# Kernel optimization log

Hardware: AMD Instinct MI355X
Metric: run time of the kernel (lower is better)

Reference implementation:

```python
import jax, jax.numpy as jnp
import numpy as np

NH, HD, MBS = 32, 64, 16   # num_heads, head_dim, mini_batch_size
BASE_LR = 1.0
ROPE_BASE = 10000.0
EPS = 1e-6


def _rotate_half(x):
    x1, x2 = jnp.split(x, 2, axis=-1)
    return jnp.concatenate((-x2, x1), axis=-1)


def _permute_qk(x):
    B, H, L, D = x.shape
    return x.reshape(B, H, L, D // 2, 2).swapaxes(-1, -2).reshape(B, H, L, D)


def _undo_permute_qk(x):
    B, H, L, D = x.shape
    return x.reshape(B, H, L, 2, D // 2).swapaxes(-1, -2).reshape(B, H, L, D)


def _ln_fwd(x, gamma, beta):
    mu = x.mean(-1, keepdims=True)
    var = x.var(-1, keepdims=True)
    return gamma * ((x - mu) / jnp.sqrt(var + EPS)) + beta


def _ln_fused_l2_bwd(x, target, gamma, beta):
    # grad of 0.5*||LN(x) - target||^2 wrt x, fused
    D = x.shape[-1]
    mu = x.mean(-1, keepdims=True)
    std = jnp.sqrt(x.var(-1, keepdims=True) + EPS)
    x_hat = (x - mu) / std
    y = gamma * x_hat + beta
    g = (y - target) * gamma
    return (D * g - g.sum(-1, keepdims=True) - x_hat * (g * x_hat).sum(-1, keepdims=True)) / (D * std)


def setup_inputs() -> dict:
    key = jax.random.key(0)
    ks = jax.random.split(key, 8)
    B, L, C, OUT = 4, 2048, 2048, 768
    s = 0.02
    return {
        "hidden_states": jax.random.normal(ks[0], (B, L, C), jnp.float32),
        "position_ids": jnp.broadcast_to(jnp.arange(L, dtype=jnp.int32)[None], (B, L)),
        "Wq": jax.random.normal(ks[1], (C, C), jnp.float32) * s,
        "Wk": jax.random.normal(ks[2], (C, C), jnp.float32) * s,
        "Wv": jax.random.normal(ks[3], (C, C), jnp.float32) * s,
        "Wo": jax.random.normal(ks[4], (C, OUT), jnp.float32) * s,
        "W1": jax.random.normal(ks[5], (NH, HD, HD), jnp.float32) * s,
        "b1": jnp.zeros((NH, 1, HD), jnp.float32),
        "ttt_lr_weight": jax.random.normal(ks[6], (NH, 1, C), jnp.float32) * s,
        "ttt_lr_bias": jnp.zeros((NH, 1), jnp.float32),
        "learnable_token_idx": jnp.zeros((MBS,), jnp.float32),
        "ttt_norm_weight": jnp.ones((NH, HD), jnp.float32),
        "ttt_norm_bias": jnp.zeros((NH, HD), jnp.float32),
        "post_norm_weight": jnp.ones((C,), jnp.float32),
        "post_norm_bias": jnp.zeros((C,), jnp.float32),
    }


def reference(hidden_states, position_ids, Wq, Wk, Wv, Wo, W1, b1,
              ttt_lr_weight, ttt_lr_bias, learnable_token_idx,
              ttt_norm_weight, ttt_norm_bias, post_norm_weight, post_norm_bias):
    B, L, C = hidden_states.shape
    NM = L // MBS
    # QKV projections -> [B, NH, L, HD]
    XQ = (hidden_states @ Wq).reshape(B, L, NH, HD).transpose(0, 2, 1, 3)
    XK = (hidden_states @ Wk).reshape(B, L, NH, HD).transpose(0, 2, 1, 3)
    XV = (hidden_states @ Wv).reshape(B, L, NH, HD).transpose(0, 2, 1, 3)
    # RoPE on positions modulo the mini-batch size
    pos = (position_ids % MBS).astype(jnp.float32)  # [B, L]
    inv_freq = 1.0 / (ROPE_BASE ** (jnp.arange(0, HD, 2, dtype=jnp.float32) / HD))
    freqs = pos[..., None] * inv_freq               # [B, L, HD/2]
    emb = jnp.concatenate((freqs, freqs), axis=-1)  # [B, L, HD]
    cos = jnp.cos(emb)[:, None]                     # [B, 1, L, HD]
    sin = jnp.sin(emb)[:, None]
    XQ, XK = _permute_qk(XQ), _permute_qk(XK)
    XQ = XQ * cos + _rotate_half(XQ) * sin
    XK = XK * cos + _rotate_half(XK) * sin
    XQ, XK = _undo_permute_qk(XQ), _undo_permute_qk(XK)
    # reshape into mini-batches: [B, NH, NM, K, HD]
    X = hidden_states.reshape(B, NM, MBS, C)
    XQ = XQ.reshape(B, NH, NM, MBS, HD)
    XK = XK.reshape(B, NH, NM, MBS, HD)
    XV = XV.reshape(B, NH, NM, MBS, HD)
    # eta: per-token learnable LR gate
    ttt_lr = jax.nn.sigmoid(
        jnp.einsum('bnkc,hdc->bhnkd', X, ttt_lr_weight)
        + ttt_lr_bias.reshape(1, NH, 1, 1, 1))              # [B,NH,NM,K,1]
    ttt_lr_eta = BASE_LR * ttt_lr.transpose(0, 1, 2, 4, 3) / HD  # [B,NH,NM,1,K]
    token_idx = jnp.clip(1.0 / jnp.arange(1, MBS + 1, dtype=jnp.float32)
                         + learnable_token_idx, 0.0, None)
    token_eta = token_idx.reshape(1, 1, 1, MBS, 1)
    eta = token_eta * ttt_lr_eta                            # [B,NH,NM,K,K]
    # TTT-Linear dual-form mini-batch scan
    ln_w = ttt_norm_weight.reshape(1, NH, 1, HD)
    ln_b = ttt_norm_bias.reshape(1, NH, 1, HD)
    W1_0 = jnp.broadcast_to(W1[None], (B, NH, HD, HD))
    b1_0 = jnp.broadcast_to(b1[None], (B, NH, 1, HD))
    tril = jnp.tril(jnp.ones((MBS, MBS), hidden_states.dtype))

    def step(carry, xs):
        W1_s, b1_s = carry
        xq, xk, xv, eta_m = xs                 # [B,NH,K,HD], eta_m [B,NH,K,K]
        Z1 = xk @ W1_s + b1_s
        target = xv - xk
        grad = _ln_fused_l2_bwd(Z1, target, ln_w, ln_b)
        Attn = tril * (xq @ xk.swapaxes(-1, -2))
        b1_bar = b1_s - (tril * eta_m) @ grad
        Z1_bar = xq @ W1_s - (eta_m * Attn) @ grad + b1_bar
        last_eta = eta_m[:, :, -1, :, None]    # [B,NH,K,1]
        W1_new = W1_s - (last_eta * xk).swapaxes(-1, -2) @ grad
        b1_new = b1_s - jnp.sum(last_eta * grad, axis=-2, keepdims=True)
        out = xq + _ln_fwd(Z1_bar, ln_w, ln_b)
        return (W1_new, b1_new), out

    xs = (XQ.transpose(2, 0, 1, 3, 4), XK.transpose(2, 0, 1, 3, 4),
          XV.transpose(2, 0, 1, 3, 4), eta.transpose(2, 0, 1, 3, 4))
    _, outs = jax.lax.scan(step, (W1_0, b1_0), xs)   # [NM,B,NH,K,HD]
    out = outs.transpose(1, 2, 0, 3, 4).reshape(B, NH, L, HD)
    out = out.transpose(0, 2, 1, 3).reshape(B, L, C)
    # post LayerNorm (eps 1e-6) and output projection
    mu = out.mean(-1, keepdims=True)
    var = out.var(-1, keepdims=True)
    out = (out - mu) / jnp.sqrt(var + EPS) * post_norm_weight + post_norm_bias
    return out @ Wo
```

## Files before the change

### kernel.cpp

```cpp
#include <hip/hip_runtime.h>
#include <cstddef>
#include <cstdint>

#define B_DIM   4
#define L_SEQ   2048
#define C_DIM   2048
#define OUT_DIM 768
#define NHEADS  32
#define HDIM    64
#define MBS_    16
#define NMINI   128
#define EPS_    1e-6f

typedef _Float16 half8 __attribute__((ext_vector_type(8)));
typedef _Float16 half4 __attribute__((ext_vector_type(4)));
typedef float floatx4 __attribute__((ext_vector_type(4)));

__device__ __forceinline__ void glds16(const void* g, void* l) {
    __builtin_amdgcn_global_load_lds(
        (const __attribute__((address_space(1))) uint32_t*)g,
        (__attribute__((address_space(3))) uint32_t*)l, 16, 0, 0);
}

__device__ __forceinline__ void split8(const float4 a, const float4 b,
                                       half8& hi, half8& lo) {
    const float x[8] = {a.x, a.y, a.z, a.w, b.x, b.y, b.z, b.w};
#pragma unroll
    for (int e = 0; e < 8; e++) {
        const _Float16 h = (_Float16)x[e];
        hi[e] = h;
        lo[e] = (_Float16)(x[e] - (float)h);
    }
}

__device__ __forceinline__ void split4(const float4 a, half4& hi, half4& lo) {
    const float x[4] = {a.x, a.y, a.z, a.w};
#pragma unroll
    for (int e = 0; e < 4; e++) {
        const _Float16 h = (_Float16)x[e];
        hi[e] = h;
        lo[e] = (_Float16)(x[e] - (float)h);
    }
}

__device__ __forceinline__ uint32_t pack_hl(float v) {
    const _Float16 h = (_Float16)v;
    const _Float16 l = (_Float16)(v - (float)h);
    union { _Float16 f[2]; uint32_t u; } p;
    p.f[0] = h; p.f[1] = l;
    return p.u;
}

__device__ __forceinline__ half8 pairswap(half8 v) {
    union { half8 h; uint32_t u[4]; } a, b;
    a.h = v;
#pragma unroll
    for (int e = 0; e < 4; e++) b.u[e] = (a.u[e] >> 16) | (a.u[e] << 16);
    return b.h;
}

template<int CTRL>
__device__ __forceinline__ float dpp_add(float v) {
    const int x = __builtin_amdgcn_update_dpp(0, __float_as_int(v), CTRL, 0xF, 0xF, false);
    return v + __int_as_float(x);
}
__device__ __forceinline__ float red16(float v) {
    v = dpp_add<0xB1>(v);
    v = dpp_add<0x4E>(v);
    v = dpp_add<0x124>(v);
    v = dpp_add<0x128>(v);
    return v;
}

__device__ __forceinline__ void bar_lgkm() {
    asm volatile("s_waitcnt lgkmcnt(0)\n\ts_barrier" ::: "memory");
}

__global__ __launch_bounds__(256)
void asplit_kernel(const float* __restrict__ A, _Float16* __restrict__ Ahi,
                   _Float16* __restrict__ Alo)
{
    const size_t idx = ((size_t)blockIdx.x * 256 + threadIdx.x) * 16;
    half8 h0, l0, h1, l1;
    {
        const float4 a = *(const float4*)(A + idx);
        const float4 b = *(const float4*)(A + idx + 4);
        split8(a, b, h0, l0);
    }
    {
        const float4 a = *(const float4*)(A + idx + 8);
        const float4 b = *(const float4*)(A + idx + 12);
        split8(a, b, h1, l1);
    }
    *(half8*)(Ahi + idx)     = h0;
    *(half8*)(Ahi + idx + 8) = h1;
    *(half8*)(Alo + idx)     = l0;
    *(half8*)(Alo + idx + 8) = l1;
}

template<int APRE>
__global__ __launch_bounds__(256)
void gemm_t(const float* __restrict__ A32,
            const _Float16* __restrict__ Ahi, const _Float16* __restrict__ Alo,
            const _Float16* __restrict__ Bhi, const _Float16* __restrict__ Blo,
            float* __restrict__ Cout, int mode, int doRope)
{
    __shared__ __align__(16) float    sA[APRE ? 1 : 4096];
    __shared__ __align__(16) _Float16 sAh[APRE ? 4096 : 1];
    __shared__ __align__(16) _Float16 sAl[APRE ? 4096 : 1];
    __shared__ __align__(16) _Float16 sBhi[4096];
    __shared__ __align__(16) _Float16 sBlo[4096];
    const int tid = threadIdx.x;
    const int nwg = gridDim.x * gridDim.y;
    int lin = blockIdx.y * gridDim.x + blockIdx.x;
    lin = (lin & 7) * (nwg >> 3) + (lin >> 3);
    const int m0 = (lin / gridDim.x) * 128;
    const int n0 = (lin % gridDim.x) * 128;
    const int K = 2048;

    size_t gA[4]; float* lA[4];
    size_t gAs[2]; _Float16 *lAh[2], *lAl[2];
    if constexpr (!APRE) {
#pragma unroll
        for (int I = 0; I < 4; I++) {
            const int c = I * 256 + tid;
            const int row = c >> 3, seg = (c & 7) ^ (row & 7);
            gA[I] = (size_t)(m0 + row) * K + seg * 4;
            lA[I] = &sA[c * 4];
        }
    } else {
#pragma unroll
        for (int I = 0; I < 2; I++) {
            const int c = I * 256 + tid;
            const int row = c >> 2, seg = (c & 3) ^ ((row >> 1) & 3);
            gAs[I] = (size_t)(m0 + row) * K + seg * 8;
            lAh[I] = &sAh[c * 8];
            lAl[I] = &sAl[c * 8];
        }
    }
    size_t gB[2]; _Float16 *lBh[2], *lBl[2];
#pragma unroll
    for (int I = 0; I < 2; I++) {
        const int c = I * 256 + tid;
        const int row = c >> 2, seg = (c & 3) ^ ((row >> 1) & 3);
        gB[I] = (size_t)(n0 + row) * K + seg * 8;
        lBh[I] = &sBhi[c * 8];
        lBl[I] = &sBlo[c * 8];
    }

    const int lane = tid & 63, quad = lane >> 4, lc = lane & 15;
    const int wv = tid >> 6, wm = wv & 1, wn = wv >> 1;
    int offA0[4], offA1[4], offAp[4], offB[4];
#pragma unroll
    for (int i = 0; i < 4; i++) {
        const int rA = wm * 64 + i * 16 + lc;
        if constexpr (!APRE) {
            offA0[i] = (rA * 8 + ((2 * quad)     ^ (rA & 7))) * 4;
            offA1[i] = (rA * 8 + ((2 * quad + 1) ^ (rA & 7))) * 4;
        } else {
            offAp[i] = (rA * 4 + (quad ^ ((rA >> 1) & 3))) * 8;
        }
    }
#pragma unroll
    for (int j = 0; j < 4; j++) {
        const int rB = wn * 64 + j * 16 + lc;
        offB[j] = (rB * 4 + (quad ^ ((rB >> 1) & 3))) * 8;
    }

    floatx4 acc[4][4];
#pragma unroll
    for (int i = 0; i < 4; i++)
#pragma unroll
        for (int j = 0; j < 4; j++) acc[i][j] = (floatx4)0.0f;

    for (int k0 = 0; k0 < K; k0 += 32) {
        __syncthreads();
        if constexpr (!APRE) {
#pragma unroll
            for (int I = 0; I < 4; I++) glds16(A32 + gA[I] + k0, lA[I]);
        } else {
#pragma unroll
            for (int I = 0; I < 2; I++) {
                glds16(Ahi + gAs[I] + k0, lAh[I]);
                glds16(Alo + gAs[I] + k0, lAl[I]);
            }
        }
#pragma unroll
        for (int I = 0; I < 2; I++) {
            glds16(Bhi + gB[I] + k0, lBh[I]);
            glds16(Blo + gB[I] + k0, lBl[I]);
        }
        __syncthreads();

        half8 ah[4], al[4], bh[4], bl[4];
#pragma unroll
        for (int i = 0; i < 4; i++) {
            if constexpr (!APRE) {
                const float4 va = *(const float4*)&sA[offA0[i]];
                const float4 vb = *(const float4*)&sA[offA1[i]];
                split8(va, vb, ah[i], al[i]);
            } else {
                ah[i] = *(const half8*)&sAh[offAp[i]];
                al[i] = *(const half8*)&sAl[offAp[i]];
            }
        }
#pragma unroll
        for (int j = 0; j < 4; j++) {
            bh[j] = *(const half8*)&sBhi[offB[j]];
            bl[j] = *(const half8*)&sBlo[offB[j]];
        }
#pragma unroll
        for (int i = 0; i < 4; i++)
#pragma unroll
            for (int j = 0; j < 4; j++) {
                acc[i][j] = __builtin_amdgcn_mfma_f32_16x16x32_f16(ah[i], bh[j], acc[i][j], 0, 0, 0);
                acc[i][j] = __builtin_amdgcn_mfma_f32_16x16x32_f16(ah[i], bl[j], acc[i][j], 0, 0, 0);
                acc[i][j] = __builtin_amdgcn_mfma_f32_16x16x32_f16(al[i], bh[j], acc[i][j], 0, 0, 0);
            }
    }

    float cs[4][4], sn[4][4];
    if (doRope) {
#pragma unroll
        for (int j = 0; j < 4; j++) {
            const int ii = ((j * 16 + lc) & 63) >> 1;
            const float invf = expf(-(float)ii * 0.28782313662425574f);
#pragma unroll
            for (int r = 0; r < 4; r++) {
                const float ang = (float)(quad * 4 + r) * invf;
                sincosf(ang, &sn[j][r], &cs[j][r]);
            }
        }
    }
    const int oddcol = lc & 1;
#pragma unroll
    for (int i = 0; i < 4; i++) {
#pragma unroll
        for (int j = 0; j < 4; j++) {
            floatx4 v = acc[i][j];
            if (doRope) {
#pragma unroll
                for (int r = 0; r < 4; r++) {
                    const float partner = __shfl_xor(v[r], 1);
                    v[r] = v[r] * cs[j][r] + partner * (oddcol ? sn[j][r] : -sn[j][r]);
                }
            }
            const int n = n0 + wn * 64 + j * 16 + lc;
            if (mode == 0) {
                const int h = (n >> 6) & 31, d = n & 63;
#pragma unroll
                for (int r = 0; r < 4; r++) {
                    const int m = m0 + wm * 64 + i * 16 + quad * 4 + r;
                    const int b = m >> 11, li = m & 2047;
                    Cout[((size_t)(b * 32 + h) * 2048 + li) * 64 + d] = v[r];
                }
            } else {
#pragma unroll
                for (int r = 0; r < 4; r++) {
                    const int m = m0 + wm * 64 + i * 16 + quad * 4 + r;
                    Cout[(size_t)m * OUT_DIM + n] = v[r];
                }
            }
        }
    }
}

__global__ __launch_bounds__(256)
void wtrans_kernel(const float* __restrict__ W, _Float16* __restrict__ BThi,
                   _Float16* __restrict__ BTlo, int Nw)
{
    __shared__ float tile[32][33];
    const int t = threadIdx.x, tx = t & 31, ty = t >> 5;
    const int n0 = blockIdx.x * 32, k0 = blockIdx.y * 32;
    const int K = 2048;
#pragma unroll
    for (int r = 0; r < 4; r++)
        tile[ty + r * 8][tx] = W[(size_t)(k0 + ty + r * 8) * Nw + n0 + tx];
    __syncthreads();
#pragma unroll
    for (int r = 0; r < 4; r++) {
        const float val = tile[tx][ty + r * 8];
        const _Float16 hh = (_Float16)val;
        const size_t o = (size_t)(n0 + ty + r * 8) * K + k0 + tx;
        BThi[o] = hh;
        BTlo[o] = (_Float16)(val - (float)hh);
    }
}

__global__ __launch_bounds__(256)
void lr_kernel(const float* __restrict__ hidden, const float* __restrict__ wlr,
               const float* __restrict__ lr_bias, float* __restrict__ lrs)
{
    __shared__ float sRow[2048];
    __shared__ float sPart[32][9];
    const int m = blockIdx.x;
    const int t = threadIdx.x;
    const float* row = hidden + (size_t)m * C_DIM;
#pragma unroll
    for (int j = 0; j < 8; j++) sRow[t + j * 256] = row[t + j * 256];
    __syncthreads();
    const int h = t >> 3, p = t & 7;
    const float* w = wlr + (size_t)h * C_DIM;
    float s = 0.0f;
#pragma unroll 8
    for (int k = 0; k < 64; k++) {
        const int c = k * 32 + p * 4;
        const float4 a = *(const float4*)(sRow + c);
        const float4 b = *(const float4*)(w + c);
        s += a.x * b.x + a.y * b.y + a.z * b.z + a.w * b.w;
    }
    sPart[h][p] = s;
    __syncthreads();
    if (t < 32) {
        float v = 0.0f;
#pragma unroll
        for (int p2 = 0; p2 < 8; p2++) v += sPart[t][p2];
        v += lr_bias[t];
        const float sig = 1.0f / (1.0f + expf(-v));
        lrs[((size_t)(m >> 11) * NHEADS + t) * L_SEQ + (m & 2047)] = sig;
    }
}

__global__ __launch_bounds__(256, 1)
void scan_mfma(const float* __restrict__ XQ, const float* __restrict__ XK,
               float* __restrict__ XVo, const float* __restrict__ LRS,
               const float* __restrict__ W1i, const float* __restrict__ b1i,
               const float* __restrict__ lt, const float* __restrict__ lnw,
               const float* __restrict__ lnb)
{
    __shared__ __align__(16) _Float16 sXqH[1024], sXqL[1024];
    __shared__ __align__(16) _Float16 sXkH[1024], sXkL[1024];
    __shared__ __align__(16) float    sTgt[16 * 68];
    __shared__ __align__(16) float    sXq32[2][16 * 68];
    __shared__ __align__(16) _Float16 sW1H[4096], sW1L[4096];
    __shared__ __align__(16) uint32_t sKT[64 * 20];
    __shared__ __align__(16) uint32_t sCf[16 * 20];
    __shared__ __align__(16) float sRedA[16 * 36];
    __shared__ __align__(16) float sRedC[16 * 12];
    __shared__ __align__(16) float sEta[16];
    __shared__ float sB1[64];

    const int bh = blockIdx.x, h = bh & 31;
    const int t = threadIdx.x;
    const int lane = t & 63, q = lane >> 4, lc = lane & 15;
    const int w = t >> 6;
    const int col = w * 16 + lc;
    const int iRow = t >> 4;
    const int m = t & 15;

    if (t < 64) sB1[t] = b1i[h * 64 + t];

    float w1s[4][4];
#pragma unroll
    for (int t4 = 0; t4 < 4; t4++)
#pragma unroll
        for (int r = 0; r < 4; r++) {
            const float v = W1i[h * 4096 + (16 * t4 + lc) * 64 + (16 * w + 4 * q + r)];
            w1s[t4][r] = v;
            const int nn = 16 * w + 4 * q + r, k = 16 * t4 + lc;
            const int off = nn * 64 + ((((k >> 3) ^ (nn & 7)) << 3) | (k & 7));
            const _Float16 hh = (_Float16)v;
            sW1H[off] = hh; sW1L[off] = (_Float16)(v - (float)hh);
        }

    const float gamC = lnw[h * 64 + col], betC = lnb[h * 64 + col];
    const float g2c = gamC * gamC;
    float sumG2 = 0.0f;
#pragma unroll
    for (int d0 = 0; d0 < 16; d0++) {
        const float4 gv = *(const float4*)(lnw + h * 64 + d0 * 4);
        sumG2 += gv.x * gv.x + gv.y * gv.y + gv.z * gv.z + gv.w * gv.w;
    }
    float tokR[4];
#pragma unroll
    for (int r = 0; r < 4; r++)
        tokR[r] = fmaxf(1.0f / (float)(4 * q + r + 1) + lt[4 * q + r], 0.0f);
    const float tok15 = fmaxf(1.0f / 16.0f + lt[15], 0.0f);

    __syncthreads();

    const size_t base = (size_t)bh * L_SEQ * HDIM;
    const float* xq_g = XQ + base;
    const float* xk_g = XK + base;
    float* xv_g = XVo + base;
    const float* lr_g = LRS + (size_t)bh * L_SEQ;

    float4 cq = *(const float4*)(xq_g + t * 4);
    float4 ck = *(const float4*)(xk_g + t * 4);
    float4 cv = *(const float4*)(xv_g + t * 4);
    float clr = lr_g[m];

    const int rw = 16 * w + lc;
    const int stOff = iRow * 64 + ((((m >> 1) ^ (iRow & 7)) << 3) | ((m & 1) << 2));
    const int gkm = (m ^ (m >> 2)) & 3;
    const int ktWb = 4 * (w ^ gkm) + q;

    for (int n = 0; n < NMINI; n++) {
        const int buf = n & 1;
        {
            half4 hq, lq, hk, lk;
            split4(cq, hq, lq);
            split4(ck, hk, lk);
            *(half4*)&sXqH[stOff] = hq;
            *(half4*)&sXqL[stOff] = lq;
            *(half4*)&sXkH[stOff] = hk;
            *(half4*)&sXkL[stOff] = lk;
            const float4 tg = make_float4(cv.x - ck.x, cv.y - ck.y,
                                          cv.z - ck.z, cv.w - ck.w);
            *(float4*)&sTgt[iRow * 68 + m * 4] = tg;
            *(float4*)&sXq32[buf][iRow * 68 + m * 4] = cq;
            const float kvv[4] = {ck.x, ck.y, ck.z, ck.w};
#pragma unroll
            for (int i2 = 0; i2 < 4; i2++)
                sKT[(4 * m + i2) * 20 + ktWb] = pack_hl(kvv[i2]);
        }
        if (t < 16) sEta[t] = clr * (1.0f / 64.0f);
        const int np = (n + 1) & (NMINI - 1);
        const float4 nq = *(const float4*)(xq_g + np * 1024 + t * 4);
        const float4 nk = *(const float4*)(xk_g + np * 1024 + t * 4);
        const float4 nv = *(const float4*)(xv_g + np * 1024 + t * 4);
        const float nlr = lr_g[np * 16 + m];
        bar_lgkm();

        const float b1c = sB1[col];
        const float4 ev = *(const float4*)&sEta[4 * q];
        const float evv[4] = {ev.x, ev.y, ev.z, ev.w};

        half8 qh[2], ql[2], kh[2], kl[2], wh[2], wl[2];
#pragma unroll
        for (int f = 0; f < 2; f++) {
            const int cx = ((4 * f + q) ^ (lc & 7)) << 3;
            qh[f] = *(const half8*)&sXqH[lc * 64 + cx];
            ql[f] = *(const half8*)&sXqL[lc * 64 + cx];
            kh[f] = *(const half8*)&sXkH[lc * 64 + cx];
            kl[f] = *(const half8*)&sXkL[lc * 64 + cx];
            const int cw = ((4 * f + q) ^ (rw & 7)) << 3;
            wh[f] = *(const half8*)&sW1H[rw * 64 + cw];
            wl[f] = *(const half8*)&sW1L[rw * 64 + cw];
        }

        floatx4 z1a = (floatx4)0.0f, zba = (floatx4)0.0f, at = (floatx4)0.0f;
#pragma unroll
        for (int f = 0; f < 2; f++) {
            z1a = __builtin_amdgcn_mfma_f32_16x16x32_f16(kh[f], wh[f], z1a, 0, 0, 0);
            z1a = __builtin_amdgcn_mfma_f32_16x16x32_f16(kh[f], wl[f], z1a, 0, 0, 0);
            z1a = __builtin_amdgcn_mfma_f32_16x16x32_f16(kl[f], wh[f], z1a, 0, 0, 0);
            zba = __builtin_amdgcn_mfma_f32_16x16x32_f16(qh[f], wh[f], zba, 0, 0, 0);
            zba = __builtin_amdgcn_mfma_f32_16x16x32_f16(qh[f], wl[f], zba, 0, 0, 0);
            zba = __builtin_amdgcn_mfma_f32_16x16x32_f16(ql[f], wh[f], zba, 0, 0, 0);
        }
        if (w == 0) {
            const float etaLC = sEta[lc];
#pragma unroll
            for (int f = 0; f < 2; f++) {
                at = __builtin_amdgcn_mfma_f32_16x16x32_f16(qh[f], kh[f], at, 0, 0, 0);
                at = __builtin_amdgcn_mfma_f32_16x16x32_f16(qh[f], kl[f], at, 0, 0, 0);
                at = __builtin_amdgcn_mfma_f32_16x16x32_f16(ql[f], kh[f], at, 0, 0, 0);
            }
#pragma unroll
            for (int r = 0; r < 4; r++) {
                const int i = 4 * q + r;
                const float cfv = (lc <= i) ? -tokR[r] * etaLC * (at[r] + 1.0f) : 0.0f;
                sCf[i * 20 + 4 * ((lc >> 2) ^ q) + (lc & 3)] = pack_hl(cfv);
            }
        }

        float z[4], cE[4];
        float sz[4], szz[4], sgz[4], sgzz[4], sc[4], scz[4];
#pragma unroll
        for (int r = 0; r < 4; r++) {
            const int row = 4 * q + r;
            z[r] = z1a[r] + b1c;
            const float tgt = sTgt[row * 68 + col];
            cE[r] = gamC * (betC - tgt);
            const float zz = z[r] * z[r];
            sz[r]   = red16(z[r]);
            szz[r]  = red16(zz);
            sgz[r]  = red16(g2c * z[r]);
            sgzz[r] = red16(g2c * zz);
            sc[r]   = red16(cE[r]);
            scz[r]  = red16(cE[r] * z[r]);
        }
        if (lc == 0) {
#pragma unroll
            for (int r = 0; r < 4; r++) {
                const int rb = (4 * q + r) * 36;
                sRedA[rb + 0  + w] = sz[r];
                sRedA[rb + 4  + w] = szz[r];
                sRedA[rb + 8  + w] = sgz[r];
                sRedA[rb + 12 + w] = sgzz[r];
                sRedA[rb + 16 + w] = sc[r];
                sRedA[rb + 20 + w] = scz[r];
            }
        }
        bar_lgkm();

        half8 ktp[4];
#pragma unroll
        for (int t4 = 0; t4 < 4; t4++) {
            const int gkr = ((lc >> 2) ^ t4) & 3;
            ktp[t4] = *(const half8*)&sKT[(16 * t4 + lc) * 20 + 4 * (q ^ gkr)];
        }
        const half8 cfp = *(const half8*)&sCf[lc * 20 + 4 * (q ^ (lc >> 2))];

        float gr[4];
#pragma unroll
        for (int r = 0; r < 4; r++) {
            const int rb = (4 * q + r) * 36;
            const float4 a0 = *(const float4*)&sRedA[rb + 0];
            const float4 a1 = *(const float4*)&sRedA[rb + 4];
            const float4 a2 = *(const float4*)&sRedA[rb + 8];
            const float4 a3 = *(const float4*)&sRedA[rb + 12];
            const float4 a4 = *(const float4*)&sRedA[rb + 16];
            const float4 a5 = *(const float4*)&sRedA[rb + 20];
            const float Sz   = a0.x + a0.y + a0.z + a0.w;
            const float Szz  = a1.x + a1.y + a1.z + a1.w;
            const float Sgz  = a2.x + a2.y + a2.z + a2.w;
            const float Sgzz = a3.x + a3.y + a3.z + a3.w;
            const float Sc   = a4.x + a4.y + a4.z + a4.w;
            const float Scz  = a5.x + a5.y + a5.z + a5.w;
            const float mu  = Sz * (1.0f / 64.0f);
            const float ex2 = Szz * (1.0f / 64.0f);
            const float rs  = rsqrtf(ex2 - mu * mu + EPS_);
            const float G1 = rs * (Sgz - mu * sumG2) + Sc;
            const float G2 = rs * rs * (Sgzz - 2.0f * mu * Sgz + mu * mu * sumG2)
                           + rs * (Scz - mu * Sc);
            const float xh = (z[r] - mu) * rs;
            const float g  = g2c * xh + cE[r];
            gr[r] = (64.0f * g - G1 - xh * G2) * rs * (1.0f / 64.0f);
        }

        half8 gf, gfl;
#pragma unroll
        for (int r = 0; r < 4; r++) {
            const _Float16 h0 = (_Float16)gr[r];
            gf[2 * r]     = h0;
            gf[2 * r + 1] = (_Float16)(gr[r] - (float)h0);
            const float gl = gr[r] * (tok15 * evv[r]);
            const _Float16 h1 = (_Float16)gl;
            gfl[2 * r]     = h1;
            gfl[2 * r + 1] = (_Float16)(gl - (float)h1);
        }
        const half8 gfs  = pairswap(gf);
        const half8 gfls = pairswap(gfl);

        zba = __builtin_amdgcn_mfma_f32_16x16x32_f16(cfp, gf,  zba, 0, 0, 0);
        zba = __builtin_amdgcn_mfma_f32_16x16x32_f16(cfp, gfs, zba, 0, 0, 0);
#pragma unroll
        for (int t4 = 0; t4 < 4; t4++) {
            floatx4 up = (floatx4)0.0f;
            up = __builtin_amdgcn_mfma_f32_16x16x32_f16(gfl,  ktp[t4], up, 0, 0, 0);
            up = __builtin_amdgcn_mfma_f32_16x16x32_f16(gfls, ktp[t4], up, 0, 0, 0);
#pragma unroll
            for (int r = 0; r < 4; r++) w1s[t4][r] -= up[r];
        }

        float z2[4], p1[4], p2[4];
#pragma unroll
        for (int r = 0; r < 4; r++) {
            z2[r] = zba[r] + b1c;
            p1[r] = red16(z2[r]);
            p2[r] = red16(z2[r] * z2[r]);
        }
        if (lc == 0)
#pragma unroll
            for (int r = 0; r < 4; r++) {
                const int rb = (4 * q + r) * 12;
                sRedC[rb + w]     = p1[r];
                sRedC[rb + 4 + w] = p2[r];
            }

        {
            float p = gr[0] * evv[0] + gr[1] * evv[1] + gr[2] * evv[2] + gr[3] * evv[3];
            p += __shfl_xor(p, 16);
            p += __shfl_xor(p, 32);
            if (q == 0) sB1[col] -= tok15 * p;
        }
#pragma unroll
        for (int t4 = 0; t4 < 4; t4++)
#pragma unroll
            for (int r = 0; r < 4; r++) {
                const int nn = 16 * w + 4 * q + r, k = 16 * t4 + lc;
                const int off = nn * 64 + ((((k >> 3) ^ (nn & 7)) << 3) | (k & 7));
                const float v = w1s[t4][r];
                const _Float16 hh = (_Float16)v;
                sW1H[off] = hh; sW1L[off] = (_Float16)(v - (float)hh);
            }
        bar_lgkm();

#pragma unroll
        for (int r = 0; r < 4; r++) {
            const int row = 4 * q + r;
            const float4 a = *(const float4*)&sRedC[row * 12];
            const float4 b = *(const float4*)&sRedC[row * 12 + 4];
            const float mu  = (a.x + a.y + a.z + a.w) * (1.0f / 64.0f);
            const float ex2 = (b.x + b.y + b.z + b.w) * (1.0f / 64.0f);
            const float rs  = rsqrtf(ex2 - mu * mu + EPS_);
            const float xqv = sXq32[buf][row * 68 + col];
            xv_g[n * 1024 + row * 64 + col] = xqv + gamC * ((z2[r] - mu) * rs) + betC;
        }
        cq = nq; ck = nk; cv = nv; clr = nlr;
    }
}

__global__ __launch_bounds__(256)
void postln_kernel(const float* __restrict__ Ob, const float* __restrict__ pnw,
                   const float* __restrict__ pnb, _Float16* __restrict__ XNhi,
                   _Float16* __restrict__ XNlo)
{
    const int m = blockIdx.x;
    const int b = m >> 11, l = m & 2047;
    const int t = threadIdx.x;
    float v[8];
    float s1 = 0.0f, s2 = 0.0f;
    const int c0 = t * 8;
    const int hh = c0 >> 6, d0 = c0 & 63;
    const float* bas = Ob + (size_t)b * NHEADS * L_SEQ * HDIM + (size_t)l * HDIM
                     + (size_t)hh * (L_SEQ * HDIM) + d0;
    {
        const float4 va = *(const float4*)(bas);
        const float4 vb = *(const float4*)(bas + 4);
        v[0] = va.x; v[1] = va.y; v[2] = va.z; v[3] = va.w;
        v[4] = vb.x; v[5] = vb.y; v[6] = vb.z; v[7] = vb.w;
    }
#pragma unroll
    for (int j = 0; j < 8; j++) { s1 += v[j]; s2 += v[j] * v[j]; }
#pragma unroll
    for (int o = 1; o < 64; o <<= 1) { s1 += __shfl_xor(s1, o); s2 += __shfl_xor(s2, o); }
    __shared__ float r1[4], r2[4];
    const int w = t >> 6;
    if ((t & 63) == 0) { r1[w] = s1; r2[w] = s2; }
    __syncthreads();
    s1 = r1[0] + r1[1] + r1[2] + r1[3];
    s2 = r2[0] + r2[1] + r2[2] + r2[3];
    const float mu = s1 * (1.0f / 2048.0f);
    const float var = s2 * (1.0f / 2048.0f) - mu * mu;
    const float rstd = rsqrtf(var + EPS_);
    half8 oh, ol;
#pragma unroll
    for (int j = 0; j < 8; j++) {
        const float y = (v[j] - mu) * rstd * pnw[c0 + j] + pnb[c0 + j];
        const _Float16 hy = (_Float16)y;
        oh[j] = hy;
        ol[j] = (_Float16)(y - (float)hy);
    }
    *(half8*)(XNhi + (size_t)m * C_DIM + c0) = oh;
    *(half8*)(XNlo + (size_t)m * C_DIM + c0) = ol;
}

extern "C" void kernel_launch(void* const* d_in, const int* in_sizes, int n_in,
                              void* d_out, int out_size, void* d_ws, size_t ws_size,
                              hipStream_t stream)
{
    (void)in_sizes; (void)n_in; (void)out_size;
    const float* hidden  = (const float*)d_in[0];
    const float* Wq      = (const float*)d_in[2];
    const float* Wk      = (const float*)d_in[3];
    const float* Wv      = (const float*)d_in[4];
    const float* Wo      = (const float*)d_in[5];
    const float* W1      = (const float*)d_in[6];
    const float* b1      = (const float*)d_in[7];
    const float* wlr     = (const float*)d_in[8];
    const float* lr_bias = (const float*)d_in[9];
    const float* lt      = (const float*)d_in[10];
    const float* lnw     = (const float*)d_in[11];
    const float* lnb     = (const float*)d_in[12];
    const float* pnw     = (const float*)d_in[13];
    const float* pnb     = (const float*)d_in[14];

    const size_t TEN = (size_t)B_DIM * NHEADS * L_SEQ * HDIM;
    float* XQ  = (float*)d_ws;
    float* XK  = XQ + TEN;
    float* XVo = XK + TEN;
    float* LRS = XVo + TEN;
    _Float16* Ahi = (_Float16*)(LRS + 262144);
    _Float16* Alo = Ahi + TEN;
    const size_t needBytes = (3 * TEN + 262144) * 4 + TEN * 4;
    const int useAsplit = (ws_size >= needBytes) ? 1 : 0;
    const dim3 blk(256);

    _Float16* BThi = (_Float16*)d_out;
    _Float16* BTlo = BThi + (size_t)C_DIM * C_DIM;

    lr_kernel<<<dim3(B_DIM * L_SEQ), blk, 0, stream>>>(hidden, wlr, lr_bias, LRS);
    if (useAsplit)
        asplit_kernel<<<dim3(4096), blk, 0, stream>>>(hidden, Ahi, Alo);

    const float* Wmats[3] = {Wq, Wk, Wv};
    float* outs[3] = {XQ, XK, XVo};
    for (int p = 0; p < 3; p++) {
        wtrans_kernel<<<dim3(64, 64), blk, 0, stream>>>(Wmats[p], BThi, BTlo, C_DIM);
        if (useAsplit)
            gemm_t<1><<<dim3(16, 64), blk, 0, stream>>>(nullptr, Ahi, Alo,
                                                        BThi, BTlo, outs[p],
                                                        0, (p < 2) ? 1 : 0);
        else
            gemm_t<0><<<dim3(16, 64), blk, 0, stream>>>(hidden, nullptr, nullptr,
                                                        BThi, BTlo, outs[p],
                                                        0, (p < 2) ? 1 : 0);
    }
    scan_mfma<<<dim3(B_DIM * NHEADS), blk, 0, stream>>>(XQ, XK, XVo, LRS,
                                                        W1, b1, lt, lnw, lnb);
    _Float16* XNhi = (_Float16*)XQ;
    _Float16* XNlo = XNhi + TEN;
    _Float16* WThi = (_Float16*)XVo;
    WThi = (_Float16*)XK;
    _Float16* WTlo = WThi + (size_t)OUT_DIM * C_DIM;
    postln_kernel<<<dim3(B_DIM * L_SEQ), blk, 0, stream>>>(XVo, pnw, pnb,
                                                           XNhi, XNlo);
    wtrans_kernel<<<dim3(24, 64), blk, 0, stream>>>(Wo, WThi, WTlo, OUT_DIM);
    gemm_t<1><<<dim3(6, 64), blk, 0, stream>>>(nullptr, XNhi, XNlo,
                                               WThi, WTlo, (float*)d_out, 1, 0);
}
```

Baseline: 1.401 ms.

## Add triple-buffered 256x128 split-fp16 GEMM with 512 threads for projections

Replaces the pre-split fp16 GEMM path with a new gemm8 kernel. It uses 512-thread blocks computing 256x128 tiles and a three-stage LDS ring buffer, so global-to-LDS loads for step t+2 are issued while MFMAs run on step t. It waits with explicit vmcnt and barrier instructions and raises wave priority around the MFMA block. The goal is to hide global load latency and cut the per-iteration double syncthreads, at the cost of much more LDS (about 144KB), which limits occupancy to one block per CU.

```diff
diff --git a/kernel.cpp b/kernel.cpp
--- a/kernel.cpp
+++ b/kernel.cpp
@@ -98,45 +98,189 @@
     *(half8*)(Alo + idx + 8) = l1;
 }
 
-template<int APRE>
+__global__ __launch_bounds__(512)
+void gemm8(const _Float16* __restrict__ Ahi, const _Float16* __restrict__ Alo,
+           const _Float16* __restrict__ Bhi, const _Float16* __restrict__ Blo,
+           float* __restrict__ Cout, int Ndim, int mode, int doRope)
+{
+    __shared__ __align__(16) _Float16 sAh[3][8192];
+    __shared__ __align__(16) _Float16 sAl[3][8192];
+    __shared__ __align__(16) _Float16 sBh[3][4096];
+    __shared__ __align__(16) _Float16 sBl[3][4096];
+    const int tid = threadIdx.x;
+    const int nbx = Ndim >> 7;
+    const int nwg = gridDim.x;
+    int lin = blockIdx.x;
+    lin = (lin & 7) * (nwg >> 3) + (lin >> 3);
+    const int m0 = (lin / nbx) * 256;
+    const int n0 = (lin % nbx) * 128;
+    const int K = 2048;
+
+    size_t gA[2];
+    int lA[2];
+#pragma unroll
+    for (int X = 0; X < 2; X++) {
+        const int c = X * 512 + tid;
+        const int row = c >> 2, s = c & 3;
+        const int ks = s ^ ((row >> 1) & 3);
+        gA[X] = (size_t)(m0 + row) * K + ks * 8;
+        lA[X] = c * 8;
+    }
+    size_t gB;
+    int lB;
+    {
+        const int row = tid >> 2, s = tid & 3;
+        const int ks = s ^ ((row >> 1) & 3);
+        gB = (size_t)(n0 + row) * K + ks * 8;
+        lB = tid * 8;
+    }
+
+    const int lane = tid & 63, q = lane >> 4, lc = lane & 15;
+    const int w = tid >> 6, wm = w >> 1, wn = w & 1;
+    int offA[4], offB[4];
+#pragma unroll
+    for (int i = 0; i < 4; i++) {
+        const int rA = wm * 64 + i * 16 + lc;
+        offA[i] = rA * 32 + ((q ^ ((rA >> 1) & 3)) << 3);
+    }
+#pragma unroll
+    for (int j = 0; j < 4; j++) {
+        const int rB = wn * 64 + j * 16 + lc;
+        offB[j] = rB * 32 + ((q ^ ((rB >> 1) & 3)) << 3);
+    }
+
+    floatx4 acc[4][4];
+#pragma unroll
+    for (int i = 0; i < 4; i++)
+#pragma unroll
+        for (int j = 0; j < 4; j++) acc[i][j] = (floatx4)0.0f;
+
+#define STAGE(T)                                                         \
+    {                                                                    \
+        const int b_ = (T) % 3;                                          \
+        const int ko_ = (T) * 32;                                        \
+        glds16(Ahi + gA[0] + ko_, &sAh[b_][lA[0]]);                      \
+        glds16(Alo + gA[0] + ko_, &sAl[b_][lA[0]]);                      \
+        glds16(Ahi + gA[1] + ko_, &sAh[b_][lA[1]]);                      \
+        glds16(Alo + gA[1] + ko_, &sAl[b_][lA[1]]);                      \
+        glds16(Bhi + gB + ko_,    &sBh[b_][lB]);                         \
+        glds16(Blo + gB + ko_,    &sBl[b_][lB]);                         \
+    }
+
+#define FRAGS(B_)                                                        \
+    half8 ah[4], al[4], bh[4], bl[4];                                    \
+    _Pragma("unroll")                                                    \
+    for (int i = 0; i < 4; i++) {                                        \
+        ah[i] = *(const half8*)&sAh[B_][offA[i]];                        \
+        al[i] = *(const half8*)&sAl[B_][offA[i]];                        \
+    }                                                                    \
+    _Pragma("unroll")                                                    \
+    for (int j = 0; j < 4; j++) {                                        \
+        bh[j] = *(const half8*)&sBh[B_][offB[j]];                        \
+        bl[j] = *(const half8*)&sBl[B_][offB[j]];                        \
+    }
+
+#define MFMAS                                                            \
+    __builtin_amdgcn_s_setprio(1);                                       \
+    _Pragma("unroll")                                                    \
+    for (int i = 0; i < 4; i++)                                          \
+        _Pragma("unroll")                                                \
+        for (int j = 0; j < 4; j++) {                                    \
+            acc[i][j] = __builtin_amdgcn_mfma_f32_16x16x32_f16(ah[i], bh[j], acc[i][j], 0, 0, 0); \
+            acc[i][j] = __builtin_amdgcn_mfma_f32_16x16x32_f16(ah[i], bl[j], acc[i][j], 0, 0, 0); \
+            acc[i][j] = __builtin_amdgcn_mfma_f32_16x16x32_f16(al[i], bh[j], acc[i][j], 0, 0, 0); \
+        }                                                                \
+    __builtin_amdgcn_s_setprio(0);
+
+    STAGE(0)
+    STAGE(1)
+    asm volatile("s_waitcnt vmcnt(6) lgkmcnt(0)\n\ts_barrier" ::: "memory");
+
+    for (int t = 0; t < 62; t++) {
+        const int b = t % 3;
+        FRAGS(b)
+        STAGE(t + 2)
+        MFMAS
+        asm volatile("s_waitcnt vmcnt(6) lgkmcnt(0)\n\ts_barrier" ::: "memory");
+    }
+    {
+        FRAGS(2)
+        MFMAS
+        asm volatile("s_waitcnt vmcnt(0) lgkmcnt(0)\n\ts_barrier" ::: "memory");
+    }
+    {
+        FRAGS(0)
+        MFMAS
+    }
+#undef STAGE
+#undef FRAGS
+#undef MFMAS
+
+    float cs[4][4], sn[4][4];
+    if (doRope) {
+#pragma unroll
+        for (int j = 0; j < 4; j++) {
+            const int ii = ((j * 16 + lc) & 63) >> 1;
+            const float invf = expf(-(float)ii * 0.28782313662425574f);
+#pragma unroll
+            for (int r = 0; r < 4; r++) {
+                const float ang = (float)(q * 4 + r) * invf;
+                sincosf(ang, &sn[j][r], &cs[j][r]);
+            }
+        }
+    }
+    const int oddcol = lc & 1;
+#pragma unroll
+    for (int i = 0; i < 4; i++) {
+#pragma unroll
+        for (int j = 0; j < 4; j++) {
+            floatx4 v = acc[i][j];
+            if (doRope) {
+#pragma unroll
+                for (int r = 0; r < 4; r++) {
+                    const float partner = __shfl_xor(v[r], 1);
+                    v[r] = v[r] * cs[j][r] + partner * (oddcol ? sn[j][r] : -sn[j][r]);
+                }
+            }
+            const int n = n0 + wn * 64 + j * 16 + lc;
+            if (mode == 0) {
+                const int h = (n >> 6) & 31, d = n & 63;
+#pragma unroll
+                for (int r = 0; r < 4; r++) {
+                    const int m = m0 + wm * 64 + i * 16 + q * 4 + r;
+                    const int b = m >> 11, li = m & 2047;
+                    Cout[((size_t)(b * 32 + h) * 2048 + li) * 64 + d] = v[r];
+                }
+            } else {
+#pragma unroll
+                for (int r = 0; r < 4; r++) {
+                    const int m = m0 + wm * 64 + i * 16 + q * 4 + r;
+                    Cout[(size_t)m * OUT_DIM + n] = v[r];
+                }
+            }
+        }
+    }
+}
+
 __global__ __launch_bounds__(256)
-void gemm_t(const float* __restrict__ A32,
-            const _Float16* __restrict__ Ahi, const _Float16* __restrict__ Alo,
-            const _Float16* __restrict__ Bhi, const _Float16* __restrict__ Blo,
-            float* __restrict__ Cout, int mode, int doRope)
+void gemm_f32(const float* __restrict__ A,
+              const _Float16* __restrict__ Bhi, const _Float16* __restrict__ Blo,
+              float* __restrict__ Cout, int mode, int doRope)
 {
-    __shared__ __align__(16) float    sA[APRE ? 1 : 4096];
-    __shared__ __align__(16) _Float16 sAh[APRE ? 4096 : 1];
-    __shared__ __align__(16) _Float16 sAl[APRE ? 4096 : 1];
+    __shared__ __align__(16) float    sA[4096];
     __shared__ __align__(16) _Float16 sBhi[4096];
     __shared__ __align__(16) _Float16 sBlo[4096];
     const int tid = threadIdx.x;
-    const int nwg = gridDim.x * gridDim.y;
-    int lin = blockIdx.y * gridDim.x + blockIdx.x;
-    lin = (lin & 7) * (nwg >> 3) + (lin >> 3);
-    const int m0 = (lin / gridDim.x) * 128;
-    const int n0 = (lin % gridDim.x) * 128;
+    const int m0 = blockIdx.y * 128, n0 = blockIdx.x * 128;
     const int K = 2048;
 
     size_t gA[4]; float* lA[4];
-    size_t gAs[2]; _Float16 *lAh[2], *lAl[2];
-    if constexpr (!APRE) {
-#pragma unroll
-        for (int I = 0; I < 4; I++) {
-            const int c = I * 256 + tid;
-            const int row = c >> 3, seg = (c & 7) ^ (row & 7);
-            gA[I] = (size_t)(m0 + row) * K + seg * 4;
-            lA[I] = &sA[c * 4];
-        }
-    } else {
-#pragma unroll
-        for (int I = 0; I < 2; I++) {
-            const int c = I * 256 + tid;
-            const int row = c >> 2, seg = (c & 3) ^ ((row >> 1) & 3);
-            gAs[I] = (size_t)(m0 + row) * K + seg * 8;
-            lAh[I] = &sAh[c * 8];
-            lAl[I] = &sAl[c * 8];
-        }
+#pragma unroll
+    for (int I = 0; I < 4; I++) {
+        const int c = I * 256 + tid;
+        const int row = c >> 3, seg = (c & 7) ^ (row & 7);
+        gA[I] = (size_t)(m0 + row) * K + seg * 4;
+        lA[I] = &sA[c * 4];
     }
     size_t gB[2]; _Float16 *lBh[2], *lBl[2];
 #pragma unroll
@@ -150,16 +294,12 @@
 
     const int lane = tid & 63, quad = lane >> 4, lc = lane & 15;
     const int wv = tid >> 6, wm = wv & 1, wn = wv >> 1;
-    int offA0[4], offA1[4], offAp[4], offB[4];
+    int offA0[4], offA1[4], offB[4];
 #pragma unroll
     for (int i = 0; i < 4; i++) {
         const int rA = wm * 64 + i * 16 + lc;
-        if constexpr (!APRE) {
-            offA0[i] = (rA * 8 + ((2 * quad)     ^ (rA & 7))) * 4;
-            offA1[i] = (rA * 8 + ((2 * quad + 1) ^ (rA & 7))) * 4;
-        } else {
-            offAp[i] = (rA * 4 + (quad ^ ((rA >> 1) & 3))) * 8;
-        }
+        offA0[i] = (rA * 8 + ((2 * quad)     ^ (rA & 7))) * 4;
+        offA1[i] = (rA * 8 + ((2 * quad + 1) ^ (rA & 7))) * 4;
     }
 #pragma unroll
     for (int j = 0; j < 4; j++) {
@@ -175,16 +315,8 @@
 
     for (int k0 = 0; k0 < K; k0 += 32) {
         __syncthreads();
-        if constexpr (!APRE) {
-#pragma unroll
-            for (int I = 0; I < 4; I++) glds16(A32 + gA[I] + k0, lA[I]);
-        } else {
-#pragma unroll
-            for (int I = 0; I < 2; I++) {
-                glds16(Ahi + gAs[I] + k0, lAh[I]);
-                glds16(Alo + gAs[I] + k0, lAl[I]);
-            }
-        }
+#pragma unroll
+        for (int I = 0; I < 4; I++) glds16(A + gA[I] + k0, lA[I]);
 #pragma unroll
         for (int I = 0; I < 2; I++) {
             glds16(Bhi + gB[I] + k0, lBh[I]);
@@ -195,14 +327,9 @@
         half8 ah[4], al[4], bh[4], bl[4];
 #pragma unroll
         for (int i = 0; i < 4; i++) {
-            if constexpr (!APRE) {
-                const float4 va = *(const float4*)&sA[offA0[i]];
-                const float4 vb = *(const float4*)&sA[offA1[i]];
-                split8(va, vb, ah[i], al[i]);
-            } else {
-                ah[i] = *(const half8*)&sAh[offAp[i]];
-                al[i] = *(const half8*)&sAl[offAp[i]];
-            }
+            const float4 va = *(const float4*)&sA[offA0[i]];
+            const float4 vb = *(const float4*)&sA[offA1[i]];
+            split8(va, vb, ah[i], al[i]);
         }
 #pragma unroll
         for (int j = 0; j < 4; j++) {
@@ -691,24 +818,22 @@
     for (int p = 0; p < 3; p++) {
         wtrans_kernel<<<dim3(64, 64), blk, 0, stream>>>(Wmats[p], BThi, BTlo, C_DIM);
         if (useAsplit)
-            gemm_t<1><<<dim3(16, 64), blk, 0, stream>>>(nullptr, Ahi, Alo,
-                                                        BThi, BTlo, outs[p],
-                                                        0, (p < 2) ? 1 : 0);
+            gemm8<<<dim3(512), dim3(512), 0, stream>>>(Ahi, Alo, BThi, BTlo,
+                                                       outs[p], C_DIM,
+                                                       0, (p < 2) ? 1 : 0);
         else
-            gemm_t<0><<<dim3(16, 64), blk, 0, stream>>>(hidden, nullptr, nullptr,
-                                                        BThi, BTlo, outs[p],
-                                                        0, (p < 2) ? 1 : 0);
+            gemm_f32<<<dim3(16, 64), blk, 0, stream>>>(hidden, BThi, BTlo,
+                                                       outs[p], 0, (p < 2) ? 1 : 0);
     }
     scan_mfma<<<dim3(B_DIM * NHEADS), blk, 0, stream>>>(XQ, XK, XVo, LRS,
                                                         W1, b1, lt, lnw, lnb);
     _Float16* XNhi = (_Float16*)XQ;
     _Float16* XNlo = XNhi + TEN;
-    _Float16* WThi = (_Float16*)XVo;
-    WThi = (_Float16*)XK;
+    _Float16* WThi = (_Float16*)XK;
     _Float16* WTlo = WThi + (size_t)OUT_DIM * C_DIM;
     postln_kernel<<<dim3(B_DIM * L_SEQ), blk, 0, stream>>>(XVo, pnw, pnb,
                                                            XNhi, XNlo);
     wtrans_kernel<<<dim3(24, 64), blk, 0, stream>>>(Wo, WThi, WTlo, OUT_DIM);
-    gemm_t<1><<<dim3(6, 64), blk, 0, stream>>>(nullptr, XNhi, XNlo,
-                                               WThi, WTlo, (float*)d_out, 1, 0);
-}
+    gemm8<<<dim3(192), dim3(512), 0, stream>>>(XNhi, XNlo, WThi, WTlo,
+                                               (float*)d_out, OUT_DIM, 1, 0);
+}
```

Result: no change. 1.402 ms (+0.1%).
